# Performance work log

Hardware: AMD Instinct MI355X
Metric: run time of the kernel (lower is better)

Reference implementation:

```python
import jax, jax.numpy as jnp
import numpy as np

NUM_HEADS = 8
DIM_HEAD = 128
SCALE = DIM_HEAD ** -0.5


def setup_inputs() -> dict:
    key = jax.random.key(0)
    ks = jax.random.split(key, 6)
    B, N, D = 8, 1024, 1024
    return {
        "s_v": jax.random.normal(ks[0], (B, N, D), jnp.float32),
        "s_m": jax.random.normal(ks[1], (B, N, D), jnp.float32),
        "g_l": jax.random.normal(ks[2], (B, NUM_HEADS, N, N), jnp.float32),
        "W_qkv": jax.random.normal(ks[3], (D, 3 * NUM_HEADS * DIM_HEAD), jnp.float32) * (D ** -0.5),
        "W_qk": jax.random.normal(ks[4], (D, 2 * NUM_HEADS * DIM_HEAD), jnp.float32) * (D ** -0.5),
        "W_out": jax.random.normal(ks[5], (NUM_HEADS * DIM_HEAD, D), jnp.float32) * ((NUM_HEADS * DIM_HEAD) ** -0.5),
        "b_out": jnp.zeros((D,), jnp.float32),
    }


def _split_heads(t):
    # [b, n, h*d] -> [b, h, n, d]
    b, n, hd = t.shape
    return t.reshape(b, n, NUM_HEADS, DIM_HEAD).transpose(0, 2, 1, 3)


def reference(s_v, s_m, g_l, W_qkv, W_qk, W_out, b_out):
    b, n, _ = s_v.shape
    q_v, k_v, v = [_split_heads(t) for t in jnp.split(s_v @ W_qkv, 3, axis=-1)]
    q_m, k_m = [_split_heads(t) for t in jnp.split(s_m @ W_qk, 2, axis=-1)]
    # trajectory attention probs (softmaxed) times raw value-stream scores
    p_m = jax.nn.softmax(jnp.einsum('bhid,bhjd->bhij', q_m, k_m), axis=-1)
    p_v = jnp.einsum('bhid,bhjd->bhij', q_v, k_v)
    dots = p_m * p_v * SCALE + g_l
    attn = jax.nn.softmax(dots, axis=-1)
    out = jnp.einsum('bhij,bhjd->bhid', attn, v)
    out = out.transpose(0, 2, 1, 3).reshape(b, n, NUM_HEADS * DIM_HEAD)
    return out @ W_out + b_out
```

## Files before the change

### kernel.cpp

```cpp
#include <hip/hip_runtime.h>

typedef __attribute__((ext_vector_type(8))) short short8;
typedef __attribute__((ext_vector_type(4))) unsigned short ushortx4;
typedef __attribute__((ext_vector_type(4))) float floatx4;

#define SCALE_F 0.08838834764831845f

__device__ __forceinline__ float b2f(unsigned short u) {
  union { unsigned int u; float f; } c; c.u = ((unsigned int)u) << 16; return c.f;
}
__device__ __forceinline__ unsigned short f2b(float f) {
  union { float f; unsigned int u; } c; c.f = f;
  unsigned int u = c.u;
  u += 0x7fffu + ((u >> 16) & 1u);
  return (unsigned short)(u >> 16);
}

#define GLD_LDS16(g, l)                                              \
  __builtin_amdgcn_global_load_lds(                                  \
      (const __attribute__((address_space(1))) void*)(g),            \
      (__attribute__((address_space(3))) void*)(l), 16, 0, 0)

__global__ __launch_bounds__(256) void cast_bf16_kernel(
    const float* __restrict__ x, unsigned short* __restrict__ y, int n) {
  int i = (blockIdx.x * 256 + threadIdx.x) * 4;
  if (i >= n) return;
  float4 v = *(const float4*)(x + i);
  ushortx4 o;
  o[0] = f2b(v.x); o[1] = f2b(v.y); o[2] = f2b(v.z); o[3] = f2b(v.w);
  *(ushortx4*)(y + i) = o;
}

__global__ __launch_bounds__(256) void split2_kernel(
    const float* __restrict__ x, unsigned short* __restrict__ y) {
  int idx = blockIdx.x * 256 + threadIdx.x;
  int row = idx >> 8;
  int c4 = (idx & 255) * 4;
  float4 v = *(const float4*)(x + (size_t)row * 1024 + c4);
  ushortx4 hi, lo;
  hi[0] = f2b(v.x); lo[0] = f2b(v.x - b2f(hi[0]));
  hi[1] = f2b(v.y); lo[1] = f2b(v.y - b2f(hi[1]));
  hi[2] = f2b(v.z); lo[2] = f2b(v.z - b2f(hi[2]));
  hi[3] = f2b(v.w); lo[3] = f2b(v.w - b2f(hi[3]));
  unsigned short* yr = y + (size_t)row * 2048;
  *(ushortx4*)(yr + c4) = hi;
  *(ushortx4*)(yr + 1024 + c4) = lo;
}

__global__ __launch_bounds__(256) void transpose_split_qk(
    const float* __restrict__ W, unsigned short* __restrict__ y) {
  __shared__ float tile[32][33];
  int t = threadIdx.x, tx = t & 31, ty = t >> 5;
  int n0 = blockIdx.x * 32, k0 = blockIdx.y * 32;
  for (int rr = ty; rr < 32; rr += 8)
    tile[rr][tx] = W[(size_t)(k0 + rr) * 2048 + n0 + tx];
  __syncthreads();
  for (int rr = ty; rr < 32; rr += 8) {
    float v = tile[tx][rr];
    unsigned short hi = f2b(v);
    unsigned short* yr = y + (size_t)(n0 + rr) * 2048;
    yr[k0 + tx] = hi;
    yr[1024 + k0 + tx] = hi;
  }
}

template<int MODE>
__global__ __launch_bounds__(256) void transpose_any(
    const void* __restrict__ inv, void* __restrict__ outv,
    int R, int C, int ldin, int ldout,
    long sIb, long sIh, long sOb, long sOh, int pstart) {
  int z = blockIdx.z, p = pstart + z, b = p >> 3, h = p & 7;
  size_t ioff = (size_t)(sIb * b + sIh * h);
  size_t ooff = (size_t)(sOb * b + sOh * h);
  __shared__ float tile[32][33];
  int t = threadIdx.x, tx = t & 31, ty = t >> 5;
  int c0 = blockIdx.x * 32, r0 = blockIdx.y * 32;
  for (int rr = ty; rr < 32; rr += 8) {
    size_t idx = ioff + (size_t)(r0 + rr) * ldin + (c0 + tx);
    tile[rr][tx] = (MODE == 2) ? b2f(((const unsigned short*)inv)[idx])
                               : ((const float*)inv)[idx];
  }
  __syncthreads();
  for (int rr = ty; rr < 32; rr += 8) {
    size_t idx = ooff + (size_t)(c0 + rr) * ldout + (r0 + tx);
    ((unsigned short*)outv)[idx] = f2b(tile[tx][rr]);
  }
}

template<int OUT_BF16, int ADD_BIAS>
__global__ __launch_bounds__(256) void gemm128(
    const unsigned short* __restrict__ A, const unsigned short* __restrict__ BT,
    void* __restrict__ Cv, const float* __restrict__ bias,
    int K, int lda, int ldb, int ldc,
    long sAz, long sAb, long sAh, long sBz, long sBb, long sBh,
    long sCz, long sCb, long sCh, int pstart) {
  int z = blockIdx.z, p = pstart + z, bb = p >> 3, hh = p & 7;
  A  += (size_t)(sAz * z + sAb * bb + sAh * hh);
  BT += (size_t)(sBz * z + sBb * bb + sBh * hh);
  size_t coff = (size_t)(sCz * z + sCb * bb + sCh * hh);

  __shared__ unsigned short Al[128][32];
  __shared__ unsigned short Bl[128][32];
  int t = threadIdx.x;
  int m0 = blockIdx.y * 128, n0 = blockIdx.x * 128;
  int w = t >> 6, l = t & 63;
  int wm = (w >> 1) * 64, wn = (w & 1) * 64;
  int lrow = l & 15, lq = l >> 4;
  floatx4 acc[4][4] = {};

  int srow = t >> 2, scol = (t & 3) * 8;
  const unsigned short* ga = A + (size_t)(m0 + srow) * lda + scol;
  const unsigned short* gb = BT + (size_t)(n0 + srow) * ldb + scol;
  unsigned short* la = &Al[srow][scol];
  unsigned short* lb = &Bl[srow][scol];
  size_t lda64 = (size_t)64 * lda, ldb64 = (size_t)64 * ldb;

  for (int k0 = 0; k0 < K; k0 += 32) {
    GLD_LDS16(ga + k0, la);
    GLD_LDS16(ga + lda64 + k0, la + 64 * 32);
    GLD_LDS16(gb + k0, lb);
    GLD_LDS16(gb + ldb64 + k0, lb + 64 * 32);
    __syncthreads();
    short8 af[4], bf[4];
#pragma unroll
    for (int i = 0; i < 4; i++) af[i] = *(const short8*)&Al[wm + i * 16 + lrow][lq * 8];
#pragma unroll
    for (int j = 0; j < 4; j++) bf[j] = *(const short8*)&Bl[wn + j * 16 + lrow][lq * 8];
#pragma unroll
    for (int i = 0; i < 4; i++)
#pragma unroll
      for (int j = 0; j < 4; j++)
        acc[i][j] = __builtin_amdgcn_mfma_f32_16x16x32_bf16(af[i], bf[j], acc[i][j], 0, 0, 0);
    __syncthreads();
  }
#pragma unroll
  for (int i = 0; i < 4; i++)
#pragma unroll
    for (int j = 0; j < 4; j++)
#pragma unroll
      for (int r = 0; r < 4; r++) {
        int row = m0 + wm + i * 16 + lq * 4 + r;
        int col = n0 + wn + j * 16 + lrow;
        float v = acc[i][j][r];
        if (ADD_BIAS) v += bias[col];
        size_t idx = coff + (size_t)row * ldc + col;
        if (OUT_BF16) ((unsigned short*)Cv)[idx] = f2b(v);
        else          ((float*)Cv)[idx] = v;
      }
}

template<int OUT_BF16, int ADD_BIAS>
__global__ __launch_bounds__(256) void gemm64(
    const unsigned short* __restrict__ A, const unsigned short* __restrict__ BT,
    void* __restrict__ Cv, const float* __restrict__ bias,
    int K, int lda, int ldb, int ldc,
    long sAz, long sAb, long sAh, long sBz, long sBb, long sBh,
    long sCz, long sCb, long sCh, int pstart) {
  int z = blockIdx.z, p = pstart + z, bb = p >> 3, hh = p & 7;
  A  += (size_t)(sAz * z + sAb * bb + sAh * hh);
  BT += (size_t)(sBz * z + sBb * bb + sBh * hh);
  size_t coff = (size_t)(sCz * z + sCb * bb + sCh * hh);

  __shared__ unsigned short Al[64][32];
  __shared__ unsigned short Bl[128][32];
  int t = threadIdx.x;
  int m0 = blockIdx.y * 64, n0 = blockIdx.x * 128;
  int w = t >> 6, l = t & 63;
  int wm = (w >> 1) * 32, wn = (w & 1) * 64;
  int lrow = l & 15, lq = l >> 4;
  floatx4 acc[2][4] = {};

  int srow = t >> 2, scol = (t & 3) * 8;
  const unsigned short* ga = A + (size_t)(m0 + srow) * lda + scol;
  const unsigned short* gb = BT + (size_t)(n0 + srow) * ldb + scol;
  unsigned short* la = &Al[srow][scol];
  unsigned short* lb = &Bl[srow][scol];
  size_t ldb64 = (size_t)64 * ldb;

  for (int k0 = 0; k0 < K; k0 += 32) {
    GLD_LDS16(ga + k0, la);
    GLD_LDS16(gb + k0, lb);
    GLD_LDS16(gb + ldb64 + k0, lb + 64 * 32);
    __syncthreads();
    short8 af[2], bf[4];
#pragma unroll
    for (int i = 0; i < 2; i++) af[i] = *(const short8*)&Al[wm + i * 16 + lrow][lq * 8];
#pragma unroll
    for (int j = 0; j < 4; j++) bf[j] = *(const short8*)&Bl[wn + j * 16 + lrow][lq * 8];
#pragma unroll
    for (int i = 0; i < 2; i++)
#pragma unroll
      for (int j = 0; j < 4; j++)
        acc[i][j] = __builtin_amdgcn_mfma_f32_16x16x32_bf16(af[i], bf[j], acc[i][j], 0, 0, 0);
    __syncthreads();
  }
#pragma unroll
  for (int i = 0; i < 2; i++)
#pragma unroll
    for (int j = 0; j < 4; j++)
#pragma unroll
      for (int r = 0; r < 4; r++) {
        int row = m0 + wm + i * 16 + lq * 4 + r;
        int col = n0 + wn + j * 16 + lrow;
        float v = acc[i][j][r];
        if (ADD_BIAS) v += bias[col];
        size_t idx = coff + (size_t)row * ldc + col;
        if (OUT_BF16) ((unsigned short*)Cv)[idx] = f2b(v);
        else          ((float*)Cv)[idx] = v;
      }
}

__global__ __launch_bounds__(256) void logits_prep(
    const float* __restrict__ qkf, unsigned short* __restrict__ qm,
    unsigned short* __restrict__ km, int pstart) {
  int idx = blockIdx.x * 256 + threadIdx.x;
  int z = blockIdx.y;
  int i = idx >> 5;
  int d4 = (idx & 31) * 4;
  int p = pstart + z, b = p >> 3, h = p & 7;
  const float* row = qkf + ((size_t)(b * 1024 + i)) * 2048 + h * 128;
  ushortx4 hi, lo;

  float4 q = *(const float4*)(row + d4);
  hi[0] = f2b(q.x); lo[0] = f2b(q.x - b2f(hi[0]));
  hi[1] = f2b(q.y); lo[1] = f2b(q.y - b2f(hi[1]));
  hi[2] = f2b(q.z); lo[2] = f2b(q.z - b2f(hi[2]));
  hi[3] = f2b(q.w); lo[3] = f2b(q.w - b2f(hi[3]));
  unsigned short* qr = qm + ((size_t)z * 1024 + i) * 384;
  *(ushortx4*)(qr + d4) = hi;
  *(ushortx4*)(qr + 128 + d4) = lo;
  *(ushortx4*)(qr + 256 + d4) = hi;

  float4 k = *(const float4*)(row + 1024 + d4);
  hi[0] = f2b(k.x); lo[0] = f2b(k.x - b2f(hi[0]));
  hi[1] = f2b(k.y); lo[1] = f2b(k.y - b2f(hi[1]));
  hi[2] = f2b(k.z); lo[2] = f2b(k.z - b2f(hi[2]));
  hi[3] = f2b(k.w); lo[3] = f2b(k.w - b2f(hi[3]));
  unsigned short* kr = km + ((size_t)z * 1024 + i) * 384;
  *(ushortx4*)(kr + d4) = hi;
  *(ushortx4*)(kr + 128 + d4) = hi;
  *(ushortx4*)(kr + 256 + d4) = lo;
}

__global__ __launch_bounds__(256) void softmax_combine(
    const float* __restrict__ smb, unsigned short* __restrict__ pvb,
    const float* __restrict__ g_l, int pstart) {
  int z = blockIdx.y, p = pstart + z;
  int w = threadIdx.x >> 6, l = threadIdx.x & 63;
  int i = blockIdx.x * 4 + w;
  const float* srow = smb + ((size_t)z * 1024 + i) * 1024;
  unsigned short* vrow = pvb + ((size_t)z * 1024 + i) * 1024;
  const float* grow = g_l + ((size_t)p * 1024 + i) * 1024;

  float4 s[4];
#pragma unroll
  for (int j = 0; j < 4; j++) s[j] = *(const float4*)(srow + j * 256 + l * 4);
  float mx = -3.0e38f;
#pragma unroll
  for (int j = 0; j < 4; j++)
    mx = fmaxf(mx, fmaxf(fmaxf(s[j].x, s[j].y), fmaxf(s[j].z, s[j].w)));
#pragma unroll
  for (int o = 32; o; o >>= 1) mx = fmaxf(mx, __shfl_xor(mx, o));
  float sum = 0.0f;
#pragma unroll
  for (int j = 0; j < 4; j++) {
    s[j].x = __expf(s[j].x - mx); s[j].y = __expf(s[j].y - mx);
    s[j].z = __expf(s[j].z - mx); s[j].w = __expf(s[j].w - mx);
    sum += (s[j].x + s[j].y) + (s[j].z + s[j].w);
  }
#pragma unroll
  for (int o = 32; o; o >>= 1) sum += __shfl_xor(sum, o);
  float inv = 1.0f / sum;

  float4 d[4];
#pragma unroll
  for (int j = 0; j < 4; j++) {
    ushortx4 pv = *(const ushortx4*)(vrow + j * 256 + l * 4);
    float4 g = *(const float4*)(grow + j * 256 + l * 4);
    d[j].x = s[j].x * inv * b2f(pv[0]) * SCALE_F + g.x;
    d[j].y = s[j].y * inv * b2f(pv[1]) * SCALE_F + g.y;
    d[j].z = s[j].z * inv * b2f(pv[2]) * SCALE_F + g.z;
    d[j].w = s[j].w * inv * b2f(pv[3]) * SCALE_F + g.w;
  }
  float mx2 = -3.0e38f;
#pragma unroll
  for (int j = 0; j < 4; j++)
    mx2 = fmaxf(mx2, fmaxf(fmaxf(d[j].x, d[j].y), fmaxf(d[j].z, d[j].w)));
#pragma unroll
  for (int o = 32; o; o >>= 1) mx2 = fmaxf(mx2, __shfl_xor(mx2, o));
  float sum2 = 0.0f;
#pragma unroll
  for (int j = 0; j < 4; j++) {
    d[j].x = __expf(d[j].x - mx2); d[j].y = __expf(d[j].y - mx2);
    d[j].z = __expf(d[j].z - mx2); d[j].w = __expf(d[j].w - mx2);
    sum2 += (d[j].x + d[j].y) + (d[j].z + d[j].w);
  }
#pragma unroll
  for (int o = 32; o; o >>= 1) sum2 += __shfl_xor(sum2, o);
  float inv2 = 1.0f / sum2;

#pragma unroll
  for (int j = 0; j < 4; j++) {
    ushortx4 o4;
    o4[0] = f2b(d[j].x * inv2); o4[1] = f2b(d[j].y * inv2);
    o4[2] = f2b(d[j].z * inv2); o4[3] = f2b(d[j].w * inv2);
    *(ushortx4*)(vrow + j * 256 + l * 4) = o4;
  }
}

__global__ __launch_bounds__(256) void softmax_av(
    const float* __restrict__ smb, const unsigned short* __restrict__ pvb,
    const float* __restrict__ g_l, const unsigned short* __restrict__ vt,
    unsigned short* __restrict__ ao, int pstart) {
  int z = blockIdx.y, p = pstart + z, b = p >> 3, h = p & 7;
  int m0 = blockIdx.x * 16;
  int t = threadIdx.x, w = t >> 6, l = t & 63;

  __shared__ unsigned short attn[16 * 1024];

  for (int it = 0; it < 2; it++) {
    int rA = it * 8 + w;
    int rB = rA + 4;
    const float* sAr = smb + ((size_t)z * 1024 + m0 + rA) * 1024;
    const float* sBr = smb + ((size_t)z * 1024 + m0 + rB) * 1024;
    const unsigned short* pAr = pvb + ((size_t)z * 1024 + m0 + rA) * 1024;
    const unsigned short* pBr = pvb + ((size_t)z * 1024 + m0 + rB) * 1024;
    const float* gAr = g_l + ((size_t)p * 1024 + m0 + rA) * 1024;
    const float* gBr = g_l + ((size_t)p * 1024 + m0 + rB) * 1024;

    float4 sa[4], sb[4], ga[4], gb[4];
    ushortx4 pa[4], pb[4];
#pragma unroll
    for (int j = 0; j < 4; j++) {
      sa[j] = *(const float4*)(sAr + j * 256 + l * 4);
      sb[j] = *(const float4*)(sBr + j * 256 + l * 4);
      pa[j] = *(const ushortx4*)(pAr + j * 256 + l * 4);
      pb[j] = *(const ushortx4*)(pBr + j * 256 + l * 4);
      ga[j] = *(const float4*)(gAr + j * 256 + l * 4);
      gb[j] = *(const float4*)(gBr + j * 256 + l * 4);
    }

    float suA = 0.f, suB = 0.f;
#pragma unroll
    for (int j = 0; j < 4; j++) {
      sa[j].x = __expf(sa[j].x); sa[j].y = __expf(sa[j].y);
      sa[j].z = __expf(sa[j].z); sa[j].w = __expf(sa[j].w);
      suA += (sa[j].x + sa[j].y) + (sa[j].z + sa[j].w);
      sb[j].x = __expf(sb[j].x); sb[j].y = __expf(sb[j].y);
      sb[j].z = __expf(sb[j].z); sb[j].w = __expf(sb[j].w);
      suB += (sb[j].x + sb[j].y) + (sb[j].z + sb[j].w);
    }
#pragma unroll
    for (int o = 32; o; o >>= 1) {
      suA += __shfl_xor(suA, o);
      suB += __shfl_xor(suB, o);
    }
    float invA = 1.0f / suA, invB = 1.0f / suB;

    float s2A = 0.f, s2B = 0.f;
#pragma unroll
    for (int j = 0; j < 4; j++) {
      sa[j].x = __expf(sa[j].x * invA * b2f(pa[j][0]) * SCALE_F + ga[j].x);
      sa[j].y = __expf(sa[j].y * invA * b2f(pa[j][1]) * SCALE_F + ga[j].y);
      sa[j].z = __expf(sa[j].z * invA * b2f(pa[j][2]) * SCALE_F + ga[j].z);
      sa[j].w = __expf(sa[j].w * invA * b2f(pa[j][3]) * SCALE_F + ga[j].w);
      s2A += (sa[j].x + sa[j].y) + (sa[j].z + sa[j].w);
      sb[j].x = __expf(sb[j].x * invB * b2f(pb[j][0]) * SCALE_F + gb[j].x);
      sb[j].y = __expf(sb[j].y * invB * b2f(pb[j][1]) * SCALE_F + gb[j].y);
      sb[j].z = __expf(sb[j].z * invB * b2f(pb[j][2]) * SCALE_F + gb[j].z);
      sb[j].w = __expf(sb[j].w * invB * b2f(pb[j][3]) * SCALE_F + gb[j].w);
      s2B += (sb[j].x + sb[j].y) + (sb[j].z + sb[j].w);
    }
#pragma unroll
    for (int o = 32; o; o >>= 1) {
      s2A += __shfl_xor(s2A, o);
      s2B += __shfl_xor(s2B, o);
    }
    float inv2A = 1.0f / s2A, inv2B = 1.0f / s2B;

    unsigned swA = (unsigned)(rA & 7) << 4;
    unsigned swB = (unsigned)(rB & 7) << 4;
    char* baseA = (char*)attn + rA * 2048;
    char* baseB = (char*)attn + rB * 2048;
#pragma unroll
    for (int j = 0; j < 4; j++) {
      ushortx4 oA, oB;
      oA[0] = f2b(sa[j].x * inv2A); oA[1] = f2b(sa[j].y * inv2A);
      oA[2] = f2b(sa[j].z * inv2A); oA[3] = f2b(sa[j].w * inv2A);
      *(ushortx4*)(baseA + ((unsigned)(j * 512 + l * 8) ^ swA)) = oA;
      oB[0] = f2b(sb[j].x * inv2B); oB[1] = f2b(sb[j].y * inv2B);
      oB[2] = f2b(sb[j].z * inv2B); oB[3] = f2b(sb[j].w * inv2B);
      *(ushortx4*)(baseB + ((unsigned)(j * 512 + l * 8) ^ swB)) = oB;
    }
  }
  __syncthreads();

  const unsigned short* BT = vt + (size_t)p * 131072;
  int wn = w * 32;
  int lrow = l & 15, lq = l >> 4;
  floatx4 acc[2] = {};

  unsigned abase = (unsigned)lrow * 2048;
  unsigned asw = ((unsigned)lrow & 7) << 4;
  const unsigned short* b0 = BT + (size_t)(wn + lrow) * 1024 + lq * 8;

#pragma unroll 8
  for (int ks = 0; ks < 32; ks++) {
    short8 af = *(const short8*)((char*)attn + abase +
                                 ((unsigned)(ks * 64 + lq * 16) ^ asw));
    short8 bf0 = *(const short8*)(b0 + ks * 32);
    short8 bf1 = *(const short8*)(b0 + 16 * 1024 + ks * 32);
    acc[0] = __builtin_amdgcn_mfma_f32_16x16x32_bf16(af, bf0, acc[0], 0, 0, 0);
    acc[1] = __builtin_amdgcn_mfma_f32_16x16x32_bf16(af, bf1, acc[1], 0, 0, 0);
  }

  size_t coff = (size_t)b * 1048576 + (size_t)h * 128;
#pragma unroll
  for (int j = 0; j < 2; j++)
#pragma unroll
    for (int r4 = 0; r4 < 4; r4++) {
      int row = m0 + lq * 4 + r4;
      int col = wn + j * 16 + lrow;
      ao[coff + (size_t)row * 1024 + col] = f2b(acc[j][r4]);
    }
}

extern "C" void kernel_launch(void* const* d_in, const int* in_sizes, int n_in,
                              void* d_out, int out_size, void* d_ws, size_t ws_size,
                              hipStream_t stream) {
  (void)in_sizes; (void)n_in; (void)out_size;
  const float* s_v   = (const float*)d_in[0];
  const float* s_m   = (const float*)d_in[1];
  const float* g_l   = (const float*)d_in[2];
  const float* W_qkv = (const float*)d_in[3];
  const float* W_qk  = (const float*)d_in[4];
  const float* W_out = (const float*)d_in[5];
  const float* b_out = (const float*)d_in[6];
  float* out = (float*)d_out;
  char* ws = (char*)d_ws;

  const bool big = (ws_size >= (size_t)721420288ull);

  unsigned short *sv_bf, *qm384, *km384, *wtqkv, *wtout, *qkvb, *vt, *ao,
                 *smhl, *wqk_hl, *pvb;
  float *qkf, *smb;
  if (big) {
    sv_bf  = (unsigned short*)(ws);
    wtqkv  = (unsigned short*)(ws + 16777216);
    wtout  = (unsigned short*)(ws + 23068672);
    qkvb   = (unsigned short*)(ws + 25165824);
    qkf    = (float*)         (ws + 75497472);
    vt     = (unsigned short*)(ws + 142606336);
    ao     = (unsigned short*)(ws + 159383552);
    smhl   = (unsigned short*)(ws + 176160768);
    wqk_hl = (unsigned short*)(ws + 209715200);
    qm384  = (unsigned short*)(ws + 218103808);
    km384  = (unsigned short*)(ws + 268435456);
    smb    = (float*)         (ws + 318767104);
    pvb    = (unsigned short*)(ws + 587202560);
  } else {
    sv_bf  = (unsigned short*)(ws);
    qm384  = (unsigned short*)(ws);
    wtqkv  = (unsigned short*)(ws + 16777216);
    km384  = (unsigned short*)(ws + 16777216);
    wtout  = (unsigned short*)(ws + 29360128);
    qkvb   = (unsigned short*)(ws + 31457280);
    qkf    = (float*)         (ws + 81788928);
    vt     = (unsigned short*)(ws + 148897792);
    ao     = (unsigned short*)(ws + 165675008);
    smhl   = (unsigned short*)(ws + 182452224);
    smb    = (float*)         (ws + 182452224);
    wqk_hl = (unsigned short*)(ws + 249561088);
    pvb    = (unsigned short*)(ws + 249561088);
  }

  cast_bf16_kernel<<<dim3(8192), 256, 0, stream>>>(s_v, sv_bf, 8388608);
  transpose_any<0><<<dim3(96, 32, 1), 256, 0, stream>>>(
      W_qkv, wtqkv, 1024, 3072, 3072, 1024, 0, 0, 0, 0, 0);
  transpose_any<0><<<dim3(32, 32, 1), 256, 0, stream>>>(
      W_out, wtout, 1024, 1024, 1024, 1024, 0, 0, 0, 0, 0);
  split2_kernel<<<dim3(8192), 256, 0, stream>>>(s_m, smhl);
  transpose_split_qk<<<dim3(64, 32, 1), 256, 0, stream>>>(W_qk, wqk_hl);
  gemm128<1, 0><<<dim3(24, 64, 1), 256, 0, stream>>>(
      sv_bf, wtqkv, qkvb, nullptr, 1024, 1024, 1024, 3072,
      0, 0, 0, 0, 0, 0, 0, 0, 0, 0);
  transpose_any<2><<<dim3(4, 32, 64), 256, 0, stream>>>(
      qkvb + 2048, vt, 1024, 128, 3072, 1024,
      (long)1024 * 3072, 128, (long)1048576, 131072, 0);

  if (big) {
    gemm128<1, 0><<<dim3(8, 8, 64), 256, 0, stream>>>(
        qkvb, qkvb + 1024, pvb, nullptr, 128, 3072, 3072, 1024,
        0, (long)1024 * 3072, 128, 0, (long)1024 * 3072, 128,
        (long)1048576, 0, 0, 0);
    gemm128<0, 0><<<dim3(16, 64, 1), 256, 0, stream>>>(
        smhl, wqk_hl, qkf, nullptr, 2048, 2048, 2048, 2048,
        0, 0, 0, 0, 0, 0, 0, 0, 0, 0);
    logits_prep<<<dim3(128, 64), 256, 0, stream>>>(qkf, qm384, km384, 0);
    gemm128<0, 0><<<dim3(8, 8, 64), 256, 0, stream>>>(
        qm384, km384, smb, nullptr, 384, 384, 384, 1024,
        (long)1024 * 384, 0, 0, (long)1024 * 384, 0, 0,
        (long)1048576, 0, 0, 0);
    softmax_av<<<dim3(64, 64), 256, 0, stream>>>(smb, pvb, g_l, vt, ao, 0);
  } else {
    gemm128<0, 0><<<dim3(16, 64, 1), 256, 0, stream>>>(
        smhl, wqk_hl, qkf, nullptr, 2048, 2048, 2048, 2048,
        0, 0, 0, 0, 0, 0, 0, 0, 0, 0);
    for (int c = 0; c < 4; c++) {
      int pstart = c * 16;
      logits_prep<<<dim3(128, 16), 256, 0, stream>>>(qkf, qm384, km384, pstart);
      gemm128<0, 0><<<dim3(8, 8, 16), 256, 0, stream>>>(
          qm384, km384, smb, nullptr, 384, 384, 384, 1024,
          (long)1024 * 384, 0, 0, (long)1024 * 384, 0, 0,
          (long)1048576, 0, 0, pstart);
      gemm128<1, 0><<<dim3(8, 8, 16), 256, 0, stream>>>(
          qkvb, qkvb + 1024, pvb, nullptr, 128, 3072, 3072, 1024,
          0, (long)1024 * 3072, 128, 0, (long)1024 * 3072, 128,
          (long)1048576, 0, 0, pstart);
      softmax_combine<<<dim3(256, 16), 256, 0, stream>>>(smb, pvb, g_l, pstart);
      gemm64<1, 0><<<dim3(1, 16, 16), 256, 0, stream>>>(
          pvb, vt, ao, nullptr, 1024, 1024, 1024, 1024,
          (long)1048576, 0, 0, 0, (long)1048576, 131072,
          0, (long)1048576, 128, pstart);
    }
  }
  gemm128<0, 1><<<dim3(8, 64, 1), 256, 0, stream>>>(
      ao, wtout, out, b_out, 1024, 1024, 1024, 1024,
      0, 0, 0, 0, 0, 0, 0, 0, 0, 0);
}
```

Before: 1.041 ms.

## Fuse QK logits split into GEMM epilogue, tile V layout, swizzle GEMM blocks

The s_m projection GEMM now writes the hi/lo bf16 split operands straight into the 384-wide q/k buffers, so the fp32 qkf intermediate and the separate logits_prep pass are gone. V is rearranged into 32-row k-blocks (vt2), which makes the B-operand loads in softmax_av contiguous per k-step. The QKV projection, QK and output GEMMs also use an XCD-aware block-index swizzle to improve L2 locality. The trade-off is scattered 2-byte stores in the fused epilogue, and a vt buffer layout that now differs between the big and small paths.

```diff
diff --git a/kernel.cpp b/kernel.cpp
--- a/kernel.cpp
+++ b/kernel.cpp
@@ -87,7 +87,23 @@
   }
 }
 
-template<int OUT_BF16, int ADD_BIAS>
+__global__ __launch_bounds__(256) void build_vt2(
+    const unsigned short* __restrict__ qkvb, unsigned short* __restrict__ vt2) {
+  int p = blockIdx.z, b = p >> 3, h = p & 7;
+  int kb = blockIdx.y;
+  int d0 = blockIdx.x * 32;
+  __shared__ float tile[32][33];
+  int t = threadIdx.x, tx = t & 31, ty = t >> 5;
+  const unsigned short* src = qkvb + (size_t)b * 3145728 + 2048 + (size_t)h * 128;
+  for (int kk = ty; kk < 32; kk += 8)
+    tile[kk][tx] = b2f(src[(size_t)(kb * 32 + kk) * 3072 + d0 + tx]);
+  __syncthreads();
+  unsigned short* dst = vt2 + ((size_t)(p * 32 + kb) * 128) * 32;
+  for (int dd = ty; dd < 32; dd += 8)
+    dst[(size_t)(d0 + dd) * 32 + tx] = f2b(tile[tx][dd]);
+}
+
+template<int OUT_BF16, int ADD_BIAS, int SWZ>
 __global__ __launch_bounds__(256) void gemm128(
     const unsigned short* __restrict__ A, const unsigned short* __restrict__ BT,
     void* __restrict__ Cv, const float* __restrict__ bias,
@@ -99,10 +115,19 @@
   BT += (size_t)(sBz * z + sBb * bb + sBh * hh);
   size_t coff = (size_t)(sCz * z + sCb * bb + sCh * hh);
 
+  int bx = blockIdx.x, by = blockIdx.y;
+  if (SWZ) {
+    int nx = gridDim.x;
+    int bid = by * nx + bx;
+    int cpx = (nx * gridDim.y) >> 3;
+    int s = (bid & 7) * cpx + (bid >> 3);
+    bx = s % nx; by = s / nx;
+  }
+
   __shared__ unsigned short Al[128][32];
   __shared__ unsigned short Bl[128][32];
   int t = threadIdx.x;
-  int m0 = blockIdx.y * 128, n0 = blockIdx.x * 128;
+  int m0 = by * 128, n0 = bx * 128;
   int w = t >> 6, l = t & 63;
   int wm = (w >> 1) * 64, wn = (w & 1) * 64;
   int lrow = l & 15, lq = l >> 4;
@@ -146,6 +171,79 @@
         size_t idx = coff + (size_t)row * ldc + col;
         if (OUT_BF16) ((unsigned short*)Cv)[idx] = f2b(v);
         else          ((float*)Cv)[idx] = v;
+      }
+}
+
+__global__ __launch_bounds__(256) void gemm_qk_logits(
+    const unsigned short* __restrict__ A, const unsigned short* __restrict__ BT,
+    unsigned short* __restrict__ qm, unsigned short* __restrict__ km) {
+  int bx = blockIdx.x, by = blockIdx.y;
+  {
+    int nx = gridDim.x;
+    int bid = by * nx + bx;
+    int cpx = (nx * gridDim.y) >> 3;
+    int s = (bid & 7) * cpx + (bid >> 3);
+    bx = s % nx; by = s / nx;
+  }
+
+  __shared__ unsigned short Al[128][32];
+  __shared__ unsigned short Bl[128][32];
+  int t = threadIdx.x;
+  int m0 = by * 128, n0 = bx * 128;
+  int w = t >> 6, l = t & 63;
+  int wm = (w >> 1) * 64, wn = (w & 1) * 64;
+  int lrow = l & 15, lq = l >> 4;
+  floatx4 acc[4][4] = {};
+
+  int srow = t >> 2, scol = (t & 3) * 8;
+  const unsigned short* ga = A + (size_t)(m0 + srow) * 2048 + scol;
+  const unsigned short* gb = BT + (size_t)(n0 + srow) * 2048 + scol;
+  unsigned short* la = &Al[srow][scol];
+  unsigned short* lb = &Bl[srow][scol];
+  size_t ld64 = (size_t)64 * 2048;
+
+  for (int k0 = 0; k0 < 2048; k0 += 32) {
+    GLD_LDS16(ga + k0, la);
+    GLD_LDS16(ga + ld64 + k0, la + 64 * 32);
+    GLD_LDS16(gb + k0, lb);
+    GLD_LDS16(gb + ld64 + k0, lb + 64 * 32);
+    __syncthreads();
+    short8 af[4], bf[4];
+#pragma unroll
+    for (int i = 0; i < 4; i++) af[i] = *(const short8*)&Al[wm + i * 16 + lrow][lq * 8];
+#pragma unroll
+    for (int j = 0; j < 4; j++) bf[j] = *(const short8*)&Bl[wn + j * 16 + lrow][lq * 8];
+#pragma unroll
+    for (int i = 0; i < 4; i++)
+#pragma unroll
+      for (int j = 0; j < 4; j++)
+        acc[i][j] = __builtin_amdgcn_mfma_f32_16x16x32_bf16(af[i], bf[j], acc[i][j], 0, 0, 0);
+    __syncthreads();
+  }
+#pragma unroll
+  for (int i = 0; i < 4; i++)
+#pragma unroll
+    for (int j = 0; j < 4; j++)
+#pragma unroll
+      for (int r = 0; r < 4; r++) {
+        int row = m0 + wm + i * 16 + lq * 4 + r;
+        int col = n0 + wn + j * 16 + lrow;
+        float v = acc[i][j][r];
+        unsigned short hi = f2b(v);
+        unsigned short lo = f2b(v - b2f(hi));
+        int bb2 = row >> 10, ii = row & 1023;
+        if (col < 1024) {
+          int hh2 = col >> 7, dd = col & 127;
+          unsigned short* qr =
+              qm + ((size_t)((bb2 << 3) | hh2) * 1024 + ii) * 384 + dd;
+          qr[0] = hi; qr[128] = lo; qr[256] = hi;
+        } else {
+          int c2 = col - 1024;
+          int hh2 = c2 >> 7, dd = c2 & 127;
+          unsigned short* kr =
+              km + ((size_t)((bb2 << 3) | hh2) * 1024 + ii) * 384 + dd;
+          kr[0] = hi; kr[128] = hi; kr[256] = lo;
+        }
       }
 }
 
@@ -310,7 +408,7 @@
 
 __global__ __launch_bounds__(256) void softmax_av(
     const float* __restrict__ smb, const unsigned short* __restrict__ pvb,
-    const float* __restrict__ g_l, const unsigned short* __restrict__ vt,
+    const float* __restrict__ g_l, const unsigned short* __restrict__ vt2,
     unsigned short* __restrict__ ao, int pstart) {
   int z = blockIdx.y, p = pstart + z, b = p >> 3, h = p & 7;
   int m0 = blockIdx.x * 16;
@@ -395,21 +493,21 @@
   }
   __syncthreads();
 
-  const unsigned short* BT = vt + (size_t)p * 131072;
   int wn = w * 32;
   int lrow = l & 15, lq = l >> 4;
   floatx4 acc[2] = {};
 
   unsigned abase = (unsigned)lrow * 2048;
   unsigned asw = ((unsigned)lrow & 7) << 4;
-  const unsigned short* b0 = BT + (size_t)(wn + lrow) * 1024 + lq * 8;
+  const unsigned short* b0 =
+      vt2 + (size_t)p * 131072 + (size_t)(wn + lrow) * 32 + lq * 8;
 
 #pragma unroll 8
   for (int ks = 0; ks < 32; ks++) {
     short8 af = *(const short8*)((char*)attn + abase +
                                  ((unsigned)(ks * 64 + lq * 16) ^ asw));
-    short8 bf0 = *(const short8*)(b0 + ks * 32);
-    short8 bf1 = *(const short8*)(b0 + 16 * 1024 + ks * 32);
+    short8 bf0 = *(const short8*)(b0 + ks * 4096);
+    short8 bf1 = *(const short8*)(b0 + 512 + ks * 4096);
     acc[0] = __builtin_amdgcn_mfma_f32_16x16x32_bf16(af, bf0, acc[0], 0, 0, 0);
     acc[1] = __builtin_amdgcn_mfma_f32_16x16x32_bf16(af, bf1, acc[1], 0, 0, 0);
   }
@@ -481,39 +579,38 @@
       W_out, wtout, 1024, 1024, 1024, 1024, 0, 0, 0, 0, 0);
   split2_kernel<<<dim3(8192), 256, 0, stream>>>(s_m, smhl);
   transpose_split_qk<<<dim3(64, 32, 1), 256, 0, stream>>>(W_qk, wqk_hl);
-  gemm128<1, 0><<<dim3(24, 64, 1), 256, 0, stream>>>(
+  gemm128<1, 0, 1><<<dim3(24, 64, 1), 256, 0, stream>>>(
       sv_bf, wtqkv, qkvb, nullptr, 1024, 1024, 1024, 3072,
       0, 0, 0, 0, 0, 0, 0, 0, 0, 0);
-  transpose_any<2><<<dim3(4, 32, 64), 256, 0, stream>>>(
-      qkvb + 2048, vt, 1024, 128, 3072, 1024,
-      (long)1024 * 3072, 128, (long)1048576, 131072, 0);
 
   if (big) {
-    gemm128<1, 0><<<dim3(8, 8, 64), 256, 0, stream>>>(
+    build_vt2<<<dim3(4, 32, 64), 256, 0, stream>>>(qkvb, vt);
+    gemm128<1, 0, 0><<<dim3(8, 8, 64), 256, 0, stream>>>(
         qkvb, qkvb + 1024, pvb, nullptr, 128, 3072, 3072, 1024,
         0, (long)1024 * 3072, 128, 0, (long)1024 * 3072, 128,
         (long)1048576, 0, 0, 0);
-    gemm128<0, 0><<<dim3(16, 64, 1), 256, 0, stream>>>(
-        smhl, wqk_hl, qkf, nullptr, 2048, 2048, 2048, 2048,
-        0, 0, 0, 0, 0, 0, 0, 0, 0, 0);
-    logits_prep<<<dim3(128, 64), 256, 0, stream>>>(qkf, qm384, km384, 0);
-    gemm128<0, 0><<<dim3(8, 8, 64), 256, 0, stream>>>(
+    gemm_qk_logits<<<dim3(16, 64, 1), 256, 0, stream>>>(
+        smhl, wqk_hl, qm384, km384);
+    gemm128<0, 0, 0><<<dim3(8, 8, 64), 256, 0, stream>>>(
         qm384, km384, smb, nullptr, 384, 384, 384, 1024,
         (long)1024 * 384, 0, 0, (long)1024 * 384, 0, 0,
         (long)1048576, 0, 0, 0);
     softmax_av<<<dim3(64, 64), 256, 0, stream>>>(smb, pvb, g_l, vt, ao, 0);
   } else {
-    gemm128<0, 0><<<dim3(16, 64, 1), 256, 0, stream>>>(
+    transpose_any<2><<<dim3(4, 32, 64), 256, 0, stream>>>(
+        qkvb + 2048, vt, 1024, 128, 3072, 1024,
+        (long)1024 * 3072, 128, (long)1048576, 131072, 0);
+    gemm128<0, 0, 0><<<dim3(16, 64, 1), 256, 0, stream>>>(
         smhl, wqk_hl, qkf, nullptr, 2048, 2048, 2048, 2048,
         0, 0, 0, 0, 0, 0, 0, 0, 0, 0);
     for (int c = 0; c < 4; c++) {
       int pstart = c * 16;
       logits_prep<<<dim3(128, 16), 256, 0, stream>>>(qkf, qm384, km384, pstart);
-      gemm128<0, 0><<<dim3(8, 8, 16), 256, 0, stream>>>(
+      gemm128<0, 0, 0><<<dim3(8, 8, 16), 256, 0, stream>>>(
           qm384, km384, smb, nullptr, 384, 384, 384, 1024,
           (long)1024 * 384, 0, 0, (long)1024 * 384, 0, 0,
           (long)1048576, 0, 0, pstart);
-      gemm128<1, 0><<<dim3(8, 8, 16), 256, 0, stream>>>(
+      gemm128<1, 0, 0><<<dim3(8, 8, 16), 256, 0, stream>>>(
           qkvb, qkvb + 1024, pvb, nullptr, 128, 3072, 3072, 1024,
           0, (long)1024 * 3072, 128, 0, (long)1024 * 3072, 128,
           (long)1048576, 0, 0, pstart);
@@ -524,7 +621,7 @@
           0, (long)1048576, 128, pstart);
     }
   }
-  gemm128<0, 1><<<dim3(8, 64, 1), 256, 0, stream>>>(
+  gemm128<0, 1, 1><<<dim3(8, 64, 1), 256, 0, stream>>>(
       ao, wtout, out, b_out, 1024, 1024, 1024, 1024,
       0, 0, 0, 0, 0, 0, 0, 0, 0, 0);
 }
```

After: 975.9 us. -6.2%, faster.
